# Optimization experiments

Hardware: AMD Instinct MI355X
Metric: run time of the kernel (lower is better)

Reference implementation:

```python
import jax, jax.numpy as jnp
import numpy as np

N = 100000      # nodes
E = 3200000     # edges
D = 128         # embedding_dimension
SLOPE = 0.01    # LeakyReLU default negative slope


def _linear_params(key, fan_in, fan_out):
    kw, kb = jax.random.split(key)
    s = 1.0 / np.sqrt(fan_in)
    W = jax.random.uniform(kw, (fan_in, fan_out), minval=-s, maxval=s, dtype=jnp.float32)
    b = jax.random.uniform(kb, (fan_out,), minval=-s, maxval=s, dtype=jnp.float32)
    return W, b


def setup_inputs() -> dict:
    key = jax.random.key(0)
    ks = jax.random.split(key, 16)
    inp = {
        'des': jax.random.normal(ks[0], (N, 768), dtype=jnp.float32),
        'tweet': jax.random.normal(ks[1], (N, 768), dtype=jnp.float32),
        'num_prop': jax.random.normal(ks[2], (N, 6), dtype=jnp.float32),
        'cat_prop': jax.random.normal(ks[3], (N, 11), dtype=jnp.float32),
        'edge_index': jax.random.randint(ks[4], (2, E), 0, N, dtype=jnp.int64),
        'edge_type': jax.random.randint(ks[5], (E,), 0, 3, dtype=jnp.int64),
    }
    inp['W_des'], inp['b_des'] = _linear_params(ks[6], 768, D // 4)
    inp['W_tweet'], inp['b_tweet'] = _linear_params(ks[7], 768, D // 4)
    inp['W_num'], inp['b_num'] = _linear_params(ks[8], 6, D // 4)
    inp['W_cat'], inp['b_cat'] = _linear_params(ks[9], 11, D // 4)
    inp['W_in'], inp['b_in'] = _linear_params(ks[10], D, D)
    inp['W_g1'], inp['b_g1'] = _linear_params(ks[11], D, D)
    inp['W_g2'], inp['b_g2'] = _linear_params(ks[12], D, D)
    inp['W_o1'], inp['b_o1'] = _linear_params(ks[13], D, D)
    inp['W_o2'], inp['b_o2'] = _linear_params(ks[14], D, 2)
    return inp


def _gcn_conv(x, W, b, src, dst):
    # PyG GCNConv: add self-loops, symmetric D^-1/2 (A+I) D^-1/2 normalization.
    n = x.shape[0]
    x = x @ W                                        # [N, D]
    loops = jnp.arange(n, dtype=src.dtype)
    s = jnp.concatenate([src, loops])                # [E+N]
    d = jnp.concatenate([dst, loops])                # [E+N]
    deg = jax.ops.segment_sum(jnp.ones_like(d, dtype=x.dtype), d, num_segments=n)
    dinv = jnp.where(deg > 0, jax.lax.rsqrt(deg), 0.0)
    norm = dinv[s] * dinv[d]                         # [E+N]
    msgs = norm[:, None] * x[s]                      # gather + scale
    out = jax.ops.segment_sum(msgs, d, num_segments=n)  # scatter-add
    return out + b


def reference(des, tweet, num_prop, cat_prop, edge_index, edge_type,
              W_des, b_des, W_tweet, b_tweet, W_num, b_num, W_cat, b_cat,
              W_in, b_in, W_g1, b_g1, W_g2, b_g2, W_o1, b_o1, W_o2, b_o2):
    lrelu = lambda v: jax.nn.leaky_relu(v, SLOPE)
    d = lrelu(des @ W_des + b_des)
    t = lrelu(tweet @ W_tweet + b_tweet)
    n = lrelu(num_prop @ W_num + b_num)
    c = lrelu(cat_prop @ W_cat + b_cat)
    x = jnp.concatenate([d, t, n, c], axis=1)        # [N, D]
    x = lrelu(x @ W_in + b_in)
    src, dst = edge_index[0], edge_index[1]
    x = _gcn_conv(x, W_g1, b_g1, src, dst)
    # dropout is identity in eval mode
    x = _gcn_conv(x, W_g2, b_g2, src, dst)
    x = lrelu(x @ W_o1 + b_o1)
    x = x @ W_o2 + b_o2                              # [N, 2]
    return x
```

## Files before the change

### kernel.cpp

```cpp
#include <hip/hip_runtime.h>

#define N_NODES 100000
#define N_EDGES 3200000

typedef unsigned int u32;
typedef unsigned short u16;
typedef __bf16 bf16x8 __attribute__((ext_vector_type(8)));
typedef float floatx4 __attribute__((ext_vector_type(4)));

__device__ __forceinline__ float bf2f(u16 u) { return __uint_as_float(((u32)u) << 16); }
__device__ __forceinline__ u16 f2bf(float f) {
    u32 u = __float_as_uint(f);
    u += 0x7fffu + ((u >> 16) & 1u);
    return (u16)(u >> 16);
}
__device__ __forceinline__ float lrelu(float v) { return v > 0.f ? v : 0.01f * v; }

__device__ __forceinline__ floatx4 mfma_bf16(bf16x8 a, bf16x8 b, floatx4 c) {
    return __builtin_amdgcn_mfma_f32_16x16x32_bf16(a, b, c, 0, 0, 0);
}

union bfrag { u16 u[8]; bf16x8 v; };

__device__ __forceinline__ bf16x8 pack8(float4 lo, float4 hi) {
    bfrag r;
    r.u[0] = f2bf(lo.x); r.u[1] = f2bf(lo.y); r.u[2] = f2bf(lo.z); r.u[3] = f2bf(lo.w);
    r.u[4] = f2bf(hi.x); r.u[5] = f2bf(hi.y); r.u[6] = f2bf(hi.z); r.u[7] = f2bf(hi.w);
    return r.v;
}

__global__ void k_prep(const float* Wdes, const float* Wtwt, const float* Wnum, const float* Wcat,
                       const float* Win, const float* Wg1, const float* Wg2, const float* Wo1,
                       u16* Fdes, u16* Ftwt, u16* Fnum, u16* Fcat,
                       u16* Fin, u16* Fg1, u16* Fg2, u16* Fo1) {
    int tid = blockIdx.x * 256 + threadIdx.x;
    if (tid >= 228 * 64) return;
    int t = tid >> 6, lane = tid & 63;
    int quad = lane >> 4, l16 = lane & 15;
    const float* W; u16* F; int kt, nt, Nout, Kv, fi;
    if (t < 96) {
        int u = t; W = Wdes; F = Fdes;
        if (u >= 48) { u -= 48; W = Wtwt; F = Ftwt; }
        kt = u >> 1; nt = u & 1; Nout = 32; Kv = 768; fi = kt * 2 + nt;
    } else if (t < 100) {
        int u = t - 96; W = Wnum; F = Fnum; Kv = 6;
        if (u >= 2) { u -= 2; W = Wcat; F = Fcat; Kv = 11; }
        kt = 0; nt = u; Nout = 32; fi = nt;
    } else {
        int u = t - 100;
        if (u < 32)      { W = Win; F = Fin; }
        else if (u < 64) { W = Wg1; F = Fg1; u -= 32; }
        else if (u < 96) { W = Wg2; F = Fg2; u -= 64; }
        else             { W = Wo1; F = Fo1; u -= 96; }
        kt = u >> 3; nt = u & 7; Nout = 128; Kv = 128; fi = kt * 8 + nt;
    }
    u16* dst = F + ((size_t)(fi * 64 + lane)) * 8;
    int n = nt * 16 + l16;
    for (int j = 0; j < 8; j++) {
        int k = kt * 32 + quad * 8 + j;
        dst[j] = (k < Kv) ? f2bf(W[(size_t)k * Nout + n]) : (u16)0;
    }
}

__global__ void k_hist(const int* dst, u32* cnt) {
    int e = blockIdx.x * 256 + threadIdx.x;
    atomicAdd(&cnt[dst[e]], 1u);
}

__global__ void k_dinv(const u32* cnt, float* dinv) {
    int i = blockIdx.x * 256 + threadIdx.x;
    if (i < N_NODES) dinv[i] = rsqrtf((float)(cnt[i] + 1));
}

__global__ void k_scan_a(const u32* cnt, u32* row_ptr, u32* partials) {
    __shared__ u32 s[1024];
    int i = blockIdx.x * 1024 + threadIdx.x;
    u32 v = (i < N_NODES) ? cnt[i] : 0u;
    s[threadIdx.x] = v; __syncthreads();
    for (int off = 1; off < 1024; off <<= 1) {
        u32 t = (threadIdx.x >= off) ? s[threadIdx.x - off] : 0u;
        __syncthreads(); s[threadIdx.x] += t; __syncthreads();
    }
    if (i < N_NODES) row_ptr[i] = s[threadIdx.x] - v;
    if (threadIdx.x == 1023) partials[blockIdx.x] = s[1023];
}

__global__ void k_scan_b(u32* partials) {
    __shared__ u32 s[128];
    u32 v = (threadIdx.x < 98) ? partials[threadIdx.x] : 0u;
    s[threadIdx.x] = v; __syncthreads();
    for (int off = 1; off < 128; off <<= 1) {
        u32 t = (threadIdx.x >= off) ? s[threadIdx.x - off] : 0u;
        __syncthreads(); s[threadIdx.x] += t; __syncthreads();
    }
    if (threadIdx.x < 98) partials[threadIdx.x] = s[threadIdx.x] - v;
}

__global__ void k_scan_c(u32* row_ptr, const u32* partials, u32* cursor) {
    int i = blockIdx.x * 1024 + threadIdx.x;
    if (i < N_NODES) {
        u32 r = row_ptr[i] + partials[blockIdx.x];
        row_ptr[i] = r; cursor[i] = r;
    }
}

#define FILL_K 20
#define FILL_C 625
__global__ __launch_bounds__(256) void k_fill(const int* __restrict__ src,
                                              const int* __restrict__ dst,
                                              u32* cursor, u32* col) {
    int bucket = blockIdx.x / FILL_C;
    int chunk  = blockIdx.x % FILL_C;
    int lo = bucket * (N_NODES / FILL_K);
    int hi = lo + (N_NODES / FILL_K);
    const int4* dst4 = (const int4*)dst;
    int base4 = chunk * 1280;
    for (int it = 0; it < 5; it++) {
        int i4 = base4 + it * 256 + threadIdx.x;
        int4 d = dst4[i4];
        int e = i4 * 4;
        #pragma unroll
        for (int c = 0; c < 4; c++) {
            int dv = (&d.x)[c];
            if (dv >= lo && dv < hi) {
                u32 p = atomicAdd(&cursor[dv], 1u);
                col[p] = (u32)src[e + c];
            }
        }
    }
}

__global__ __launch_bounds__(256) void k_encoder(
    const float* des, const float* twt, const float* nump, const float* catp,
    const u16* Fdes, const u16* Ftwt, const u16* Fnum, const u16* Fcat, const u16* Fin,
    const float* bdes, const float* btwt, const float* bnum, const float* bcat, const float* bin,
    const float* dinv, u16* xs) {
    __shared__ u16 h0[64][136];
    int tid = threadIdx.x, wave = tid >> 6, lane = tid & 63, quad = lane >> 4, l16 = lane & 15;
    int rowbase = blockIdx.x * 64 + wave * 16;
    int arow = min(rowbase + l16, N_NODES - 1);

    for (int m = 0; m < 2; m++) {
        const float* X = m ? twt : des;
        const u16* F = m ? Ftwt : Fdes;
        const float* B = m ? btwt : bdes;
        const float4* X4 = (const float4*)(X + (size_t)arow * 768) + quad * 2;
        floatx4 c0 = {0, 0, 0, 0}, c1 = {0, 0, 0, 0};
        float4 A0[8], A1[8];
        #pragma unroll
        for (int i = 0; i < 4; i++) {
            A0[2 * i]     = X4[i * 8];
            A0[2 * i + 1] = X4[i * 8 + 1];
        }
        #pragma unroll
        for (int g = 0; g < 6; g++) {
            #pragma unroll
            for (int i = 0; i < 4; i++) {
                int kt = (g + 1) * 4 + i;
                if (g < 5) {
                    if (g & 1) { A0[2 * i] = X4[kt * 8]; A0[2 * i + 1] = X4[kt * 8 + 1]; }
                    else       { A1[2 * i] = X4[kt * 8]; A1[2 * i + 1] = X4[kt * 8 + 1]; }
                }
            }
            #pragma unroll
            for (int i = 0; i < 4; i++) {
                int kt = g * 4 + i;
                float4 lo = (g & 1) ? A1[2 * i]     : A0[2 * i];
                float4 hi = (g & 1) ? A1[2 * i + 1] : A0[2 * i + 1];
                bf16x8 a = pack8(lo, hi);
                bf16x8 b0 = *(const bf16x8*)(F + ((size_t)((kt * 2 + 0) * 64 + lane)) * 8);
                bf16x8 b1 = *(const bf16x8*)(F + ((size_t)((kt * 2 + 1) * 64 + lane)) * 8);
                c0 = mfma_bf16(a, b0, c0);
                c1 = mfma_bf16(a, b1, c1);
            }
        }
        int cb = m * 32;
        for (int r = 0; r < 4; r++) {
            int rl = wave * 16 + quad * 4 + r;
            h0[rl][cb + l16]      = f2bf(lrelu(c0[r] + B[l16]));
            h0[rl][cb + 16 + l16] = f2bf(lrelu(c1[r] + B[16 + l16]));
        }
    }
    {
        bfrag a; bfrag a2;
        for (int j = 0; j < 8; j++) {
            int k = quad * 8 + j;
            a.u[j]  = (k < 6)  ? f2bf(nump[(size_t)arow * 6 + k])  : (u16)0;
            a2.u[j] = (k < 11) ? f2bf(catp[(size_t)arow * 11 + k]) : (u16)0;
        }
        floatx4 c0 = {0,0,0,0}, c1 = {0,0,0,0}, c2 = {0,0,0,0}, c3 = {0,0,0,0};
        bf16x8 b0 = *(const bf16x8*)(Fnum + (size_t)(0 * 64 + lane) * 8);
        bf16x8 b1 = *(const bf16x8*)(Fnum + (size_t)(1 * 64 + lane) * 8);
        bf16x8 b2 = *(const bf16x8*)(Fcat + (size_t)(0 * 64 + lane) * 8);
        bf16x8 b3 = *(const bf16x8*)(Fcat + (size_t)(1 * 64 + lane) * 8);
        c0 = mfma_bf16(a.v, b0, c0);
        c1 = mfma_bf16(a.v, b1, c1);
        c2 = mfma_bf16(a2.v, b2, c2);
        c3 = mfma_bf16(a2.v, b3, c3);
        for (int r = 0; r < 4; r++) {
            int rl = wave * 16 + quad * 4 + r;
            h0[rl][64 + l16]  = f2bf(lrelu(c0[r] + bnum[l16]));
            h0[rl][80 + l16]  = f2bf(lrelu(c1[r] + bnum[16 + l16]));
            h0[rl][96 + l16]  = f2bf(lrelu(c2[r] + bcat[l16]));
            h0[rl][112 + l16] = f2bf(lrelu(c3[r] + bcat[16 + l16]));
        }
    }
    __syncthreads();
    floatx4 acc[8];
    for (int nt = 0; nt < 8; nt++) acc[nt] = (floatx4){0, 0, 0, 0};
    for (int kt = 0; kt < 4; kt++) {
        bf16x8 a = *(const bf16x8*)&h0[wave * 16 + l16][kt * 32 + quad * 8];
        for (int nt = 0; nt < 8; nt++) {
            bf16x8 b = *(const bf16x8*)(Fin + (size_t)((kt * 8 + nt) * 64 + lane) * 8);
            acc[nt] = mfma_bf16(a, b, acc[nt]);
        }
    }
    for (int nt = 0; nt < 8; nt++)
        for (int r = 0; r < 4; r++) {
            int grow = rowbase + quad * 4 + r;
            if (grow < N_NODES) {
                float v = lrelu(acc[nt][r] + bin[nt * 16 + l16]);
                xs[(size_t)grow * 128 + nt * 16 + l16] = f2bf(dinv[grow] * v);
            }
        }
}

__global__ __launch_bounds__(256) void k_gather(const u16* xs, u16* zs, const u32* row_ptr,
                                                const u32* cnt, const float* dinv, const u32* col) {
    int wave = threadIdx.x >> 6, lane = threadIdx.x & 63;
    int node = blockIdx.x * 4 + wave;
    const u32* xr = (const u32*)xs;
    u32 self = xr[(size_t)node * 64 + lane];
    float a0 = bf2f((u16)(self & 0xffff)), a1 = bf2f((u16)(self >> 16));
    u32 start = row_ptr[node];
    u32 m = cnt[node];
    for (u32 base = 0; base < m; base += 64) {
        u32 idx = base + lane;
        int c = (idx < m) ? (int)col[start + idx] : 0;
        int kmax = (int)min(64u, m - base);
        int j = 0;
        for (; j + 8 <= kmax; j += 8) {
            u32 w[8];
            #pragma unroll
            for (int q = 0; q < 8; q++) {
                int s = __shfl(c, j + q);
                w[q] = xr[(size_t)s * 64 + lane];
            }
            #pragma unroll
            for (int q = 0; q < 8; q++) {
                a0 += bf2f((u16)(w[q] & 0xffff));
                a1 += bf2f((u16)(w[q] >> 16));
            }
        }
        for (; j < kmax; j++) {
            int s = __shfl(c, j);
            u32 w = xr[(size_t)s * 64 + lane];
            a0 += bf2f((u16)(w & 0xffff));
            a1 += bf2f((u16)(w >> 16));
        }
    }
    float dv = dinv[node];
    u32 o = (u32)f2bf(dv * a0) | ((u32)f2bf(dv * a1) << 16);
    ((u32*)zs)[(size_t)node * 64 + lane] = o;
}

__global__ __launch_bounds__(256) void k_gemm_g1(const u16* zs, const u16* Fg1, const float* bg1,
                                                 const float* dinv, u16* xs) {
    int tid = threadIdx.x, wave = tid >> 6, lane = tid & 63, quad = lane >> 4, l16 = lane & 15;
    int rowbase = blockIdx.x * 64 + wave * 16;
    int arow = min(rowbase + l16, N_NODES - 1);
    floatx4 acc[8];
    for (int nt = 0; nt < 8; nt++) acc[nt] = (floatx4){0, 0, 0, 0};
    for (int kt = 0; kt < 4; kt++) {
        bf16x8 a = *(const bf16x8*)(zs + (size_t)arow * 128 + kt * 32 + quad * 8);
        for (int nt = 0; nt < 8; nt++) {
            bf16x8 b = *(const bf16x8*)(Fg1 + (size_t)((kt * 8 + nt) * 64 + lane) * 8);
            acc[nt] = mfma_bf16(a, b, acc[nt]);
        }
    }
    for (int nt = 0; nt < 8; nt++)
        for (int r = 0; r < 4; r++) {
            int grow = rowbase + quad * 4 + r;
            if (grow < N_NODES) {
                float v = acc[nt][r] + bg1[nt * 16 + l16];
                xs[(size_t)grow * 128 + nt * 16 + l16] = f2bf(dinv[grow] * v);
            }
        }
}

__global__ __launch_bounds__(256) void k_tail(const u16* zs, const u16* Fg2, const float* bg2,
                                              const u16* Fo1, const float* bo1,
                                              const float* Wo2, const float* bo2, float* out) {
    __shared__ u16 t0[64][136];
    __shared__ float t1[64][130];
    int tid = threadIdx.x, wave = tid >> 6, lane = tid & 63, quad = lane >> 4, l16 = lane & 15;
    int rowbase = blockIdx.x * 64 + wave * 16;
    int arow = min(rowbase + l16, N_NODES - 1);
    floatx4 acc[8];
    for (int nt = 0; nt < 8; nt++) acc[nt] = (floatx4){0, 0, 0, 0};
    for (int kt = 0; kt < 4; kt++) {
        bf16x8 a = *(const bf16x8*)(zs + (size_t)arow * 128 + kt * 32 + quad * 8);
        for (int nt = 0; nt < 8; nt++) {
            bf16x8 b = *(const bf16x8*)(Fg2 + (size_t)((kt * 8 + nt) * 64 + lane) * 8);
            acc[nt] = mfma_bf16(a, b, acc[nt]);
        }
    }
    for (int nt = 0; nt < 8; nt++)
        for (int r = 0; r < 4; r++) {
            int rl = wave * 16 + quad * 4 + r;
            t0[rl][nt * 16 + l16] = f2bf(acc[nt][r] + bg2[nt * 16 + l16]);
        }
    __syncthreads();
    for (int nt = 0; nt < 8; nt++) acc[nt] = (floatx4){0, 0, 0, 0};
    for (int kt = 0; kt < 4; kt++) {
        bf16x8 a = *(const bf16x8*)&t0[wave * 16 + l16][kt * 32 + quad * 8];
        for (int nt = 0; nt < 8; nt++) {
            bf16x8 b = *(const bf16x8*)(Fo1 + (size_t)((kt * 8 + nt) * 64 + lane) * 8);
            acc[nt] = mfma_bf16(a, b, acc[nt]);
        }
    }
    for (int nt = 0; nt < 8; nt++)
        for (int r = 0; r < 4; r++) {
            int rl = wave * 16 + quad * 4 + r;
            t1[rl][nt * 16 + l16] = lrelu(acc[nt][r] + bo1[nt * 16 + l16]);
        }
    __syncthreads();
    if (tid < 128) {
        int nl = tid >> 1, j = tid & 1;
        int grow = blockIdx.x * 64 + nl;
        if (grow < N_NODES) {
            float s = bo2[j];
            for (int k = 0; k < 128; k++) s += t1[nl][k] * Wo2[k * 2 + j];
            out[(size_t)grow * 2 + j] = s;
        }
    }
}

extern "C" void kernel_launch(void* const* d_in, const int* in_sizes, int n_in,
                              void* d_out, int out_size, void* d_ws, size_t ws_size,
                              hipStream_t stream) {
    const float* des  = (const float*)d_in[0];
    const float* twt  = (const float*)d_in[1];
    const float* nump = (const float*)d_in[2];
    const float* catp = (const float*)d_in[3];
    const int* ei   = (const int*)d_in[4];
    const int* esrc = ei;
    const int* edst = ei + N_EDGES;
    const float* Wdes = (const float*)d_in[6];  const float* bdes = (const float*)d_in[7];
    const float* Wtwt = (const float*)d_in[8];  const float* btwt = (const float*)d_in[9];
    const float* Wnum = (const float*)d_in[10]; const float* bnum = (const float*)d_in[11];
    const float* Wcat = (const float*)d_in[12]; const float* bcat = (const float*)d_in[13];
    const float* Win  = (const float*)d_in[14]; const float* bin  = (const float*)d_in[15];
    const float* Wg1  = (const float*)d_in[16]; const float* bg1  = (const float*)d_in[17];
    const float* Wg2  = (const float*)d_in[18]; const float* bg2  = (const float*)d_in[19];
    const float* Wo1  = (const float*)d_in[20]; const float* bo1  = (const float*)d_in[21];
    const float* Wo2  = (const float*)d_in[22]; const float* bo2  = (const float*)d_in[23];

    char* ws = (char*)d_ws;
    size_t off = 0;
    auto alloc = [&](size_t b) { off = (off + 511) & ~(size_t)511; size_t o = off; off += b; return o; };
    u16* Fdes = (u16*)(ws + alloc(49152));
    u16* Ftwt = (u16*)(ws + alloc(49152));
    u16* Fnum = (u16*)(ws + alloc(2048));
    u16* Fcat = (u16*)(ws + alloc(2048));
    u16* Fin  = (u16*)(ws + alloc(32768));
    u16* Fg1  = (u16*)(ws + alloc(32768));
    u16* Fg2  = (u16*)(ws + alloc(32768));
    u16* Fo1  = (u16*)(ws + alloc(32768));
    u32* cnt     = (u32*)(ws + alloc((size_t)N_NODES * 4));
    float* dinv  = (float*)(ws + alloc((size_t)N_NODES * 4));
    u32* row_ptr = (u32*)(ws + alloc((size_t)(N_NODES + 1) * 4));
    u32* cursor  = (u32*)(ws + alloc((size_t)N_NODES * 4));
    u32* partials= (u32*)(ws + alloc(1024));
    u32* col     = (u32*)(ws + alloc((size_t)N_EDGES * 4));
    u16* xs      = (u16*)(ws + alloc((size_t)N_NODES * 128 * 2));
    u16* zs      = (u16*)(ws + alloc((size_t)N_NODES * 128 * 2));

    hipMemsetAsync(cnt, 0, (size_t)N_NODES * 4, stream);
    k_prep<<<57, 256, 0, stream>>>(Wdes, Wtwt, Wnum, Wcat, Win, Wg1, Wg2, Wo1,
                                   Fdes, Ftwt, Fnum, Fcat, Fin, Fg1, Fg2, Fo1);
    k_hist<<<N_EDGES / 256, 256, 0, stream>>>(edst, cnt);
    k_dinv<<<(N_NODES + 255) / 256, 256, 0, stream>>>(cnt, dinv);
    k_scan_a<<<98, 1024, 0, stream>>>(cnt, row_ptr, partials);
    k_scan_b<<<1, 128, 0, stream>>>(partials);
    k_scan_c<<<98, 1024, 0, stream>>>(row_ptr, partials, cursor);
    k_fill<<<FILL_K * FILL_C, 256, 0, stream>>>(esrc, edst, cursor, col);
    k_encoder<<<1563, 256, 0, stream>>>(des, twt, nump, catp,
                                        Fdes, Ftwt, Fnum, Fcat, Fin,
                                        bdes, btwt, bnum, bcat, bin, dinv, xs);
    k_gather<<<25000, 256, 0, stream>>>(xs, zs, row_ptr, cnt, dinv, col);
    k_gemm_g1<<<1563, 256, 0, stream>>>(zs, Fg1, bg1, dinv, xs);
    k_gather<<<25000, 256, 0, stream>>>(xs, zs, row_ptr, cnt, dinv, col);
    k_tail<<<1563, 256, 0, stream>>>(zs, Fg2, bg2, Fo1, bo1, Wo2, bo2, (float*)d_out);
}
```

Before: 1.253 ms.

## Stage encoder inputs through LDS with coalesced loads and 16-row blocks

The encoder now processes 16 rows per block instead of 64. Each half of the block cooperatively loads the des or tweet rows with fully coalesced float4 reads, converts them to bf16 and stores them in shared memory. Work is split so each wave computes one 16-column output tile for one input, and the W_in GEMM splits its N tiles across waves. The goal is to replace strided per-lane row reads with coalesced streaming and to raise parallelism across 6250 blocks, at the cost of about 50KB of LDS per block and an extra barrier. The N_NODES bound check is dropped, which is safe only because 100000 divides evenly by 16.

```diff
diff --git a/kernel.cpp b/kernel.cpp
--- a/kernel.cpp
+++ b/kernel.cpp
@@ -21,13 +21,6 @@
 }
 
 union bfrag { u16 u[8]; bf16x8 v; };
-
-__device__ __forceinline__ bf16x8 pack8(float4 lo, float4 hi) {
-    bfrag r;
-    r.u[0] = f2bf(lo.x); r.u[1] = f2bf(lo.y); r.u[2] = f2bf(lo.z); r.u[3] = f2bf(lo.w);
-    r.u[4] = f2bf(hi.x); r.u[5] = f2bf(hi.y); r.u[6] = f2bf(hi.z); r.u[7] = f2bf(hi.w);
-    return r.v;
-}
 
 __global__ void k_prep(const float* Wdes, const float* Wtwt, const float* Wnum, const float* Wcat,
                        const float* Win, const float* Wg1, const float* Wg2, const float* Wo1,
@@ -135,94 +128,93 @@
     const u16* Fdes, const u16* Ftwt, const u16* Fnum, const u16* Fcat, const u16* Fin,
     const float* bdes, const float* btwt, const float* bnum, const float* bcat, const float* bin,
     const float* dinv, u16* xs) {
-    __shared__ u16 h0[64][136];
+    __shared__ __align__(16) u16 As[2][16][776];
+    __shared__ __align__(16) u16 h0[16][136];
     int tid = threadIdx.x, wave = tid >> 6, lane = tid & 63, quad = lane >> 4, l16 = lane & 15;
-    int rowbase = blockIdx.x * 64 + wave * 16;
-    int arow = min(rowbase + l16, N_NODES - 1);
-
-    for (int m = 0; m < 2; m++) {
-        const float* X = m ? twt : des;
-        const u16* F = m ? Ftwt : Fdes;
-        const float* B = m ? btwt : bdes;
-        const float4* X4 = (const float4*)(X + (size_t)arow * 768) + quad * 2;
-        floatx4 c0 = {0, 0, 0, 0}, c1 = {0, 0, 0, 0};
-        float4 A0[8], A1[8];
+    int rowbase = blockIdx.x * 16;
+    int half = wave >> 1;
+
+    {
+        int t = tid & 127;
+        const float* X = half ? twt : des;
+        const float4* X4 = (const float4*)(X + (size_t)rowbase * 768);
         #pragma unroll
-        for (int i = 0; i < 4; i++) {
-            A0[2 * i]     = X4[i * 8];
-            A0[2 * i + 1] = X4[i * 8 + 1];
-        }
+        for (int rd = 0; rd < 3; rd++) {
+            float4 v[8];
+            #pragma unroll
+            for (int q8 = 0; q8 < 8; q8++)
+                v[q8] = X4[(rd * 8 + q8) * 128 + t];
+            #pragma unroll
+            for (int q8 = 0; q8 < 8; q8++) {
+                int f = (rd * 8 + q8) * 512 + t * 4;
+                int r = f / 768, c = f - r * 768;
+                u32 lo = (u32)f2bf(v[q8].x) | ((u32)f2bf(v[q8].y) << 16);
+                u32 hi = (u32)f2bf(v[q8].z) | ((u32)f2bf(v[q8].w) << 16);
+                *(uint2*)&As[half][r][c] = make_uint2(lo, hi);
+            }
+        }
+    }
+    __syncthreads();
+
+    {
+        const u16* F = half ? Ftwt : Fdes;
+        const float* B = half ? btwt : bdes;
+        int nt = wave & 1;
+        floatx4 c0 = {0, 0, 0, 0};
         #pragma unroll
-        for (int g = 0; g < 6; g++) {
-            #pragma unroll
-            for (int i = 0; i < 4; i++) {
-                int kt = (g + 1) * 4 + i;
-                if (g < 5) {
-                    if (g & 1) { A0[2 * i] = X4[kt * 8]; A0[2 * i + 1] = X4[kt * 8 + 1]; }
-                    else       { A1[2 * i] = X4[kt * 8]; A1[2 * i + 1] = X4[kt * 8 + 1]; }
-                }
-            }
-            #pragma unroll
-            for (int i = 0; i < 4; i++) {
-                int kt = g * 4 + i;
-                float4 lo = (g & 1) ? A1[2 * i]     : A0[2 * i];
-                float4 hi = (g & 1) ? A1[2 * i + 1] : A0[2 * i + 1];
-                bf16x8 a = pack8(lo, hi);
-                bf16x8 b0 = *(const bf16x8*)(F + ((size_t)((kt * 2 + 0) * 64 + lane)) * 8);
-                bf16x8 b1 = *(const bf16x8*)(F + ((size_t)((kt * 2 + 1) * 64 + lane)) * 8);
-                c0 = mfma_bf16(a, b0, c0);
-                c1 = mfma_bf16(a, b1, c1);
-            }
-        }
-        int cb = m * 32;
-        for (int r = 0; r < 4; r++) {
-            int rl = wave * 16 + quad * 4 + r;
-            h0[rl][cb + l16]      = f2bf(lrelu(c0[r] + B[l16]));
-            h0[rl][cb + 16 + l16] = f2bf(lrelu(c1[r] + B[16 + l16]));
-        }
-    }
-    {
-        bfrag a; bfrag a2;
+        for (int kt = 0; kt < 24; kt++) {
+            bf16x8 a = *(const bf16x8*)&As[half][l16][kt * 32 + quad * 8];
+            bf16x8 b = *(const bf16x8*)(F + ((size_t)((kt * 2 + nt) * 64 + lane)) * 8);
+            c0 = mfma_bf16(a, b, c0);
+        }
+        int cb = half * 32 + nt * 16;
+        for (int r = 0; r < 4; r++)
+            h0[quad * 4 + r][cb + l16] = f2bf(lrelu(c0[r] + B[nt * 16 + l16]));
+    }
+    if (wave < 2) {
+        int arow = rowbase + l16;
+        bfrag a;
+        const float* P = wave ? catp : nump;
+        int Kv = wave ? 11 : 6;
+        const u16* F = wave ? Fcat : Fnum;
+        const float* B = wave ? bcat : bnum;
         for (int j = 0; j < 8; j++) {
             int k = quad * 8 + j;
-            a.u[j]  = (k < 6)  ? f2bf(nump[(size_t)arow * 6 + k])  : (u16)0;
-            a2.u[j] = (k < 11) ? f2bf(catp[(size_t)arow * 11 + k]) : (u16)0;
-        }
-        floatx4 c0 = {0,0,0,0}, c1 = {0,0,0,0}, c2 = {0,0,0,0}, c3 = {0,0,0,0};
-        bf16x8 b0 = *(const bf16x8*)(Fnum + (size_t)(0 * 64 + lane) * 8);
-        bf16x8 b1 = *(const bf16x8*)(Fnum + (size_t)(1 * 64 + lane) * 8);
-        bf16x8 b2 = *(const bf16x8*)(Fcat + (size_t)(0 * 64 + lane) * 8);
-        bf16x8 b3 = *(const bf16x8*)(Fcat + (size_t)(1 * 64 + lane) * 8);
+            a.u[j] = (k < Kv) ? f2bf(P[(size_t)arow * Kv + k]) : (u16)0;
+        }
+        floatx4 c0 = {0, 0, 0, 0}, c1 = {0, 0, 0, 0};
+        bf16x8 b0 = *(const bf16x8*)(F + (size_t)(0 * 64 + lane) * 8);
+        bf16x8 b1 = *(const bf16x8*)(F + (size_t)(1 * 64 + lane) * 8);
         c0 = mfma_bf16(a.v, b0, c0);
         c1 = mfma_bf16(a.v, b1, c1);
-        c2 = mfma_bf16(a2.v, b2, c2);
-        c3 = mfma_bf16(a2.v, b3, c3);
-        for (int r = 0; r < 4; r++) {
-            int rl = wave * 16 + quad * 4 + r;
-            h0[rl][64 + l16]  = f2bf(lrelu(c0[r] + bnum[l16]));
-            h0[rl][80 + l16]  = f2bf(lrelu(c1[r] + bnum[16 + l16]));
-            h0[rl][96 + l16]  = f2bf(lrelu(c2[r] + bcat[l16]));
-            h0[rl][112 + l16] = f2bf(lrelu(c3[r] + bcat[16 + l16]));
+        int cb = 64 + wave * 32;
+        for (int r = 0; r < 4; r++) {
+            h0[quad * 4 + r][cb + l16]      = f2bf(lrelu(c0[r] + B[l16]));
+            h0[quad * 4 + r][cb + 16 + l16] = f2bf(lrelu(c1[r] + B[16 + l16]));
         }
     }
     __syncthreads();
-    floatx4 acc[8];
-    for (int nt = 0; nt < 8; nt++) acc[nt] = (floatx4){0, 0, 0, 0};
-    for (int kt = 0; kt < 4; kt++) {
-        bf16x8 a = *(const bf16x8*)&h0[wave * 16 + l16][kt * 32 + quad * 8];
-        for (int nt = 0; nt < 8; nt++) {
-            bf16x8 b = *(const bf16x8*)(Fin + (size_t)((kt * 8 + nt) * 64 + lane) * 8);
-            acc[nt] = mfma_bf16(a, b, acc[nt]);
-        }
-    }
-    for (int nt = 0; nt < 8; nt++)
+
+    {
+        int n0 = wave * 2, n1 = wave * 2 + 1;
+        floatx4 acc0 = {0, 0, 0, 0}, acc1 = {0, 0, 0, 0};
+        #pragma unroll
+        for (int ktl = 0; ktl < 4; ktl++) {
+            bf16x8 a = *(const bf16x8*)&h0[l16][ktl * 32 + quad * 8];
+            bf16x8 b0 = *(const bf16x8*)(Fin + (size_t)((ktl * 8 + n0) * 64 + lane) * 8);
+            bf16x8 b1 = *(const bf16x8*)(Fin + (size_t)((ktl * 8 + n1) * 64 + lane) * 8);
+            acc0 = mfma_bf16(a, b0, acc0);
+            acc1 = mfma_bf16(a, b1, acc1);
+        }
         for (int r = 0; r < 4; r++) {
             int grow = rowbase + quad * 4 + r;
-            if (grow < N_NODES) {
-                float v = lrelu(acc[nt][r] + bin[nt * 16 + l16]);
-                xs[(size_t)grow * 128 + nt * 16 + l16] = f2bf(dinv[grow] * v);
-            }
-        }
+            float dv = dinv[grow];
+            float v0 = lrelu(acc0[r] + bin[n0 * 16 + l16]);
+            float v1 = lrelu(acc1[r] + bin[n1 * 16 + l16]);
+            xs[(size_t)grow * 128 + n0 * 16 + l16] = f2bf(dv * v0);
+            xs[(size_t)grow * 128 + n1 * 16 + l16] = f2bf(dv * v1);
+        }
+    }
 }
 
 __global__ __launch_bounds__(256) void k_gather(const u16* xs, u16* zs, const u32* row_ptr,
@@ -385,7 +377,7 @@
     k_scan_b<<<1, 128, 0, stream>>>(partials);
     k_scan_c<<<98, 1024, 0, stream>>>(row_ptr, partials, cursor);
     k_fill<<<FILL_K * FILL_C, 256, 0, stream>>>(esrc, edst, cursor, col);
-    k_encoder<<<1563, 256, 0, stream>>>(des, twt, nump, catp,
+    k_encoder<<<6250, 256, 0, stream>>>(des, twt, nump, catp,
                                         Fdes, Ftwt, Fnum, Fcat, Fin,
                                         bdes, btwt, bnum, bcat, bin, dinv, xs);
     k_gather<<<25000, 256, 0, stream>>>(xs, zs, row_ptr, cnt, dinv, col);
```

New measurement: 1.222 ms. 2.5% less time.
